# Kernel tuning notes

Measured on AMD Instinct MI355X. Metric: run time of the kernel, lower is better.

Reference implementation:

```python
import jax, jax.numpy as jnp
import numpy as np

DECAY = 0.99
EPS = 1e-5
K = 32  # cluster_size


def setup_inputs() -> dict:
    key = jax.random.key(0)
    k1, k2 = jax.random.split(key)
    B, D, L = 64, 256, 4096
    x = jax.random.normal(k1, (B, D, L), dtype=jnp.float32)
    embed = jax.random.normal(k2, (D, K), dtype=jnp.float32)  # [output_dim, cluster_size]
    cluster_number = jnp.zeros((K,), dtype=jnp.float32)
    embed_avg = embed  # registered buffer initialized as embed.clone()
    return {"x": x, "embed": embed, "cluster_number": cluster_number,
            "embed_avg": embed_avg, "training": 1}


def reference(x, embed, cluster_number, embed_avg, training):
    D = embed.shape[0]
    xt = jnp.transpose(x, (0, 2, 1))          # [B, L, D]
    flatten = xt.reshape(-1, D)               # [N, D]
    # squared L2 distance to each code: ||f||^2 - 2 f.e + ||e||^2
    dist = ((flatten * flatten).sum(1, keepdims=True)
            - 2.0 * flatten @ embed
            + (embed * embed).sum(0, keepdims=True))  # [N, K]
    emb_ind = jnp.argmin(dist, axis=1)        # [N]
    quantize = jnp.take(embed.T, emb_ind, axis=0).reshape(xt.shape)  # [B, L, D]

    if training:
        # EMA codebook update (one-hot sums expressed as segment sums)
        counts = jax.ops.segment_sum(jnp.ones_like(emb_ind, dtype=flatten.dtype),
                                     emb_ind, num_segments=K)          # [K]
        embed_sum = jax.ops.segment_sum(flatten, emb_ind, num_segments=K).T  # [D, K]
        cluster_number = DECAY * cluster_number + (1.0 - DECAY) * counts
        embed_avg = DECAY * embed_avg + (1.0 - DECAY) * embed_sum
        n = cluster_number.sum()
        cn = (cluster_number + EPS) / (n + K * EPS) * n
        embed_out = embed_avg / cn[None, :]
    else:
        embed_out = embed

    discrete_loss = jnp.mean((jax.lax.stop_gradient(quantize) - xt) ** 2)
    quantize = xt + jax.lax.stop_gradient(quantize - xt)  # straight-through
    return jnp.transpose(quantize, (0, 2, 1)), embed_out, discrete_loss
```

## Files before the change

kernel.cpp:

```cpp
#include <hip/hip_runtime.h>


constexpr int   Kc  = 32;
constexpr int   Dc  = 256;
constexpr int   Bc  = 64;
constexpr int   Lc  = 4096;
constexpr int   Nc  = Bc * Lc;
constexpr long  QSIZE = (long)Bc * Dc * Lc;
constexpr float DECAYf = 0.99f;
constexpr float EPSf   = 1e-5f;
constexpr float GAP_THRESH = 0.02f;

constexpr int DCH = 16;
constexpr int NCH = Dc / DCH;

typedef float f32x4 __attribute__((ext_vector_type(4)));

constexpr int WS_LOSS   = 0;
constexpr int WS_COUNTS = 8;
constexpr int NREPC     = 8;
constexpr int WS_ESUM   = 512;

#define WAITVM(N) asm volatile("s_waitcnt vmcnt(" #N ")" ::: "memory")

__device__ __forceinline__ void bar() {
    asm volatile("s_waitcnt lgkmcnt(0)" ::: "memory");
    __builtin_amdgcn_s_barrier();
}

__device__ __forceinline__ void async_ld16(const float* g, float* l) {
    __builtin_amdgcn_global_load_lds(
        (const __attribute__((address_space(1))) void*)g,
        (__attribute__((address_space(3))) void*)l, 16, 0, 0);
}

__device__ __forceinline__ void stage_chunk(const float* xt, int c,
                                            float* sbuf, int tid) {
    const float* g0 = xt + (size_t)(c * DCH) * Lc;
#pragma unroll
    for (int q = 0; q < 4; ++q) {
        const int i4 = q * 256 + tid;
        async_ld16(g0 + (size_t)(i4 >> 6) * Lc + ((i4 & 63) << 2),
                   sbuf + (size_t)i4 * 4);
    }
}

constexpr int SACC    = 4096;
constexpr int SACC_LD = 257;
constexpr int POOLF   = SACC + Kc * SACC_LD;

__global__ __launch_bounds__(256, 3) void vq_main(
    const float* __restrict__ x, const float* __restrict__ embed,
    float* __restrict__ out_q, float* __restrict__ ws, int nrep)
{
    __shared__ float  s_pool[POOLF];
    __shared__ float  s_esq[Kc];
    __shared__ double s_esqd[Kc];
    __shared__ float  s_hist[Kc];
    __shared__ float  s_red[4];
    __shared__ int    s_k[256];

    const int tid = threadIdx.x;
    const int p0  = blockIdx.x * 256;
    const int b   = p0 >> 12;
    const int l0  = p0 & (Lc - 1);
    const float* xt = x + (size_t)b * Dc * Lc + l0;

    stage_chunk(xt, 0, s_pool, tid);

    if (tid < Kc) {
        s_hist[tid] = 0.f;
        double acc = 0.0;
        for (int d = 0; d < Dc; ++d) {
            double e = (double)embed[d * Kc + tid];
            acc = fma(e, e, acc);
        }
        s_esqd[tid] = acc;
        s_esq[tid]  = (float)acc;
    }

    float dot[Kc];
#pragma unroll
    for (int k = 0; k < Kc; ++k) dot[k] = 0.f;
    float xsq = 0.f;

    for (int c = 0; c < NCH; ++c) {
        const int cb = c & 1;
        if (c + 1 < NCH) {
            stage_chunk(xt, c + 1, s_pool + (cb ^ 1) * 4096, tid);
            WAITVM(4);
        } else {
            WAITVM(0);
        }
        bar();
        const float* er0 = embed + c * DCH * Kc;
        const float* sx  = s_pool + cb * 4096;
#pragma unroll
        for (int dd = 0; dd < DCH; ++dd) {
            const float f = sx[dd * 256 + tid];
            xsq = fmaf(f, f, xsq);
            const float* er = er0 + dd * Kc;
#pragma unroll
            for (int k = 0; k < Kc; ++k) dot[k] = fmaf(f, er[k], dot[k]);
        }
        bar();
    }

#pragma unroll
    for (int k = 0; k < Kc; ++k) s_pool[SACC + k * SACC_LD + tid] = 0.f;

    int   kstar  = 0;
    float best   = 3.4e38f;
    float second = 3.4e38f;
#pragma unroll
    for (int k = 0; k < Kc; ++k) {
        float cc = fmaf(-2.0f, dot[k], s_esq[k]);
        if (cc < best)        { second = best; best = cc; kstar = k; }
        else if (cc < second) { second = cc; }
    }

    if (second - best < GAP_THRESH) {
        const float lim = best + GAP_THRESH;
        double bestd = 1e300;
        int kb = 0;
        for (int k = 0; k < Kc; ++k) {
            float cf = fmaf(-2.0f, dot[k], s_esq[k]);
            if (__any(cf <= lim)) {
                double acc = 0.0;
                for (int d = 0; d < Dc; ++d)
                    acc = fma((double)xt[(size_t)d * Lc + tid],
                              (double)embed[d * Kc + k], acc);
                double cc = fma(-2.0, acc, s_esqd[k]);
                if (cc < bestd) { bestd = cc; kb = k; }
            }
        }
        kstar = kb;
    }

    s_k[tid] = kstar;
    atomicAdd(&s_hist[kstar], 1.0f);

    float lacc = best + xsq;
#pragma unroll
    for (int off = 32; off > 0; off >>= 1) lacc += __shfl_down(lacc, off);
    if ((tid & 63) == 0) s_red[tid >> 6] = lacc;
    bar();

    const int repc = blockIdx.x & (NREPC - 1);
    if (tid == 0)
        atomicAdd(&ws[WS_LOSS], s_red[0] + s_red[1] + s_red[2] + s_red[3]);
    if (tid < Kc)
        atomicAdd(&ws[WS_COUNTS + repc * Kc + tid], s_hist[tid]);

    const int rep = blockIdx.x & (nrep - 1);
    float* esum = ws + WS_ESUM + (size_t)rep * Dc * Kc;
    float* ot   = out_q + (size_t)b * Dc * Lc + l0;
    const int w     = tid >> 6;
    const int lane  = tid & 63;
    const int dd_own = tid >> 4;
    const int s_own  = tid & 15;

    int k4[4];
#pragma unroll
    for (int t = 0; t < 4; ++t) k4[t] = s_k[(lane << 2) + t];
    int kk[16];
#pragma unroll
    for (int j = 0; j < 16; ++j) kk[j] = s_k[j * 16 + s_own];

    float* s_acc = s_pool + SACC;

    for (int c = 0; c < NCH; ++c) {
        stage_chunk(xt, c, s_pool, tid);

#pragma unroll
        for (int j = 0; j < 4; ++j) {
            const int d = c * DCH + (j << 2) + w;
            const float* erow = embed + d * Kc;
            f32x4 q;
            q.x = erow[k4[0]];
            q.y = erow[k4[1]];
            q.z = erow[k4[2]];
            q.w = erow[k4[3]];
            __builtin_nontemporal_store(
                q, reinterpret_cast<f32x4*>(ot + (size_t)d * Lc + (lane << 2)));
        }
        WAITVM(0);
        bar();

#pragma unroll
        for (int j = 0; j < 16; ++j) {
            const float f = s_pool[dd_own * 256 + j * 16 + s_own];
            s_acc[kk[j] * SACC_LD + tid] += f;
        }
        bar();

#pragma unroll
        for (int t = 0; t < 2; ++t) {
            const int j2  = (t << 8) + tid;
            const int kc  = j2 & 31;
            const int ddc = j2 >> 5;
            float ssum = 0.f;
#pragma unroll
            for (int s = 0; s < 16; ++s) {
                float* cell = &s_acc[kc * SACC_LD + ddc * 16 + s];
                ssum += *cell;
                *cell = 0.f;
            }
            atomicAdd(&esum[(size_t)(c * DCH + ddc) * Kc + kc], ssum);
        }
        bar();
    }
}

__global__ void vq_finalize(
    const float* __restrict__ embed,
    const float* __restrict__ cluster_number,
    const float* __restrict__ embed_avg,
    const int*   __restrict__ training,
    const float* __restrict__ ws,
    float* __restrict__ out, int nrep)
{
    const int j = blockIdx.x * 256 + threadIdx.x;
    if (j >= Dc * Kc) return;
    const int k = j & (Kc - 1);

    float n = 0.f, cn_k = 0.f;
    for (int kk = 0; kk < Kc; ++kk) {
        float c = 0.f;
        for (int r = 0; r < NREPC; ++r) c += ws[WS_COUNTS + r * Kc + kk];
        float cnew = DECAYf * cluster_number[kk] + (1.0f - DECAYf) * c;
        n += cnew;
        if (kk == k) cn_k = cnew;
    }
    float cn = (cn_k + EPSf) / (n + Kc * EPSf) * n;

    float s = 0.f;
    for (int r = 0; r < nrep; ++r) s += ws[WS_ESUM + (size_t)r * Dc * Kc + j];
    float avg = DECAYf * embed_avg[j] + (1.0f - DECAYf) * s;

    out[QSIZE + j] = (*training) ? (avg / cn) : embed[j];

    if (j == 0) {
        out[QSIZE + Dc * Kc] = ws[WS_LOSS] / (float)QSIZE;
    }
}

extern "C" void kernel_launch(void* const* d_in, const int* in_sizes, int n_in,
                              void* d_out, int out_size, void* d_ws, size_t ws_size,
                              hipStream_t stream)
{
    (void)in_sizes; (void)n_in; (void)out_size;
    const float* x              = (const float*)d_in[0];
    const float* embed          = (const float*)d_in[1];
    const float* cluster_number = (const float*)d_in[2];
    const float* embed_avg      = (const float*)d_in[3];
    const int*   training       = (const int*)d_in[4];
    float* out = (float*)d_out;
    float* ws  = (float*)d_ws;

    const size_t availf = ws_size / 4;
    int nrep = 8;
    while (nrep < 128 &&
           (size_t)WS_ESUM + (size_t)(nrep << 1) * Dc * Kc <= availf)
        nrep <<= 1;

    const size_t used = ((size_t)WS_ESUM + (size_t)nrep * Dc * Kc) * 4;
    (void)hipMemsetAsync(d_ws, 0, used, stream);
    vq_main<<<Nc / 256, 256, 0, stream>>>(x, embed, out, ws, nrep);
    vq_finalize<<<(Dc * Kc + 255) / 256, 256, 0, stream>>>(
        embed, cluster_number, embed_avg, training, ws, out, nrep);
}
```

Before: 628.3 us.

## Restructure scatter pass: direct global x reads, byte-packed indices, smaller LDS for occupancy

The second pass over x no longer stages chunks into LDS asynchronously. Each thread now reads float4 vectors of x straight from global memory and scatters them into the per-code LDS accumulator, working on 32-dim chunks. Code indices are stored as bytes and packed four per dword, which shrinks LDS use and register pressure, and launch bounds rise to 4 blocks per CU. This also drops one barrier per chunk. The risks are uncoalesced-ish direct global reads and a smaller replication count (nrep capped at 64), which means more atomic contention.

```diff
diff --git a/kernel.cpp b/kernel.cpp
--- a/kernel.cpp
+++ b/kernel.cpp
@@ -13,6 +13,8 @@
 
 constexpr int DCH = 16;
 constexpr int NCH = Dc / DCH;
+constexpr int DCH2 = 32;
+constexpr int NCH2 = Dc / DCH2;
 
 typedef float f32x4 __attribute__((ext_vector_type(4)));
 
@@ -45,11 +47,10 @@
     }
 }
 
-constexpr int SACC    = 4096;
 constexpr int SACC_LD = 257;
-constexpr int POOLF   = SACC + Kc * SACC_LD;
-
-__global__ __launch_bounds__(256, 3) void vq_main(
+constexpr int POOLF   = Kc * SACC_LD;
+
+__global__ __launch_bounds__(256, 4) void vq_main(
     const float* __restrict__ x, const float* __restrict__ embed,
     float* __restrict__ out_q, float* __restrict__ ws, int nrep)
 {
@@ -58,7 +59,7 @@
     __shared__ double s_esqd[Kc];
     __shared__ float  s_hist[Kc];
     __shared__ float  s_red[4];
-    __shared__ int    s_k[256];
+    __shared__ unsigned char s_k8[256] __attribute__((aligned(4)));
 
     const int tid = threadIdx.x;
     const int p0  = blockIdx.x * 256;
@@ -107,7 +108,7 @@
     }
 
 #pragma unroll
-    for (int k = 0; k < Kc; ++k) s_pool[SACC + k * SACC_LD + tid] = 0.f;
+    for (int k = 0; k < Kc; ++k) s_pool[k * SACC_LD + tid] = 0.f;
 
     int   kstar  = 0;
     float best   = 3.4e38f;
@@ -137,7 +138,7 @@
         kstar = kb;
     }
 
-    s_k[tid] = kstar;
+    s_k8[tid] = (unsigned char)kstar;
     atomicAdd(&s_hist[kstar], 1.0f);
 
     float lacc = best + xsq;
@@ -155,58 +156,59 @@
     const int rep = blockIdx.x & (nrep - 1);
     float* esum = ws + WS_ESUM + (size_t)rep * Dc * Kc;
     float* ot   = out_q + (size_t)b * Dc * Lc + l0;
-    const int w     = tid >> 6;
-    const int lane  = tid & 63;
-    const int dd_own = tid >> 4;
-    const int s_own  = tid & 15;
-
-    int k4[4];
-#pragma unroll
-    for (int t = 0; t < 4; ++t) k4[t] = s_k[(lane << 2) + t];
-    int kk[16];
-#pragma unroll
-    for (int j = 0; j < 16; ++j) kk[j] = s_k[j * 16 + s_own];
-
-    float* s_acc = s_pool + SACC;
-
-    for (int c = 0; c < NCH; ++c) {
-        stage_chunk(xt, c, s_pool, tid);
-
-#pragma unroll
-        for (int j = 0; j < 4; ++j) {
-            const int d = c * DCH + (j << 2) + w;
+    const int w    = tid >> 6;
+    const int lane = tid & 63;
+    const int dd   = tid >> 3;
+    const int s    = tid & 7;
+
+    const unsigned int k4dw =
+        *reinterpret_cast<const unsigned int*>(s_k8 + 4 * lane);
+    unsigned int kdw[8];
+#pragma unroll
+    for (int j4 = 0; j4 < 8; ++j4)
+        kdw[j4] = *reinterpret_cast<const unsigned int*>(s_k8 + 32 * j4 + 4 * s);
+
+    float* s_acc = s_pool;
+
+    for (int c = 0; c < NCH2; ++c) {
+#pragma unroll
+        for (int j = 0; j < 8; ++j) {
+            const int d = c * DCH2 + (j << 2) + w;
             const float* erow = embed + d * Kc;
             f32x4 q;
-            q.x = erow[k4[0]];
-            q.y = erow[k4[1]];
-            q.z = erow[k4[2]];
-            q.w = erow[k4[3]];
+            q.x = erow[k4dw & 255];
+            q.y = erow[(k4dw >> 8) & 255];
+            q.z = erow[(k4dw >> 16) & 255];
+            q.w = erow[k4dw >> 24];
             __builtin_nontemporal_store(
                 q, reinterpret_cast<f32x4*>(ot + (size_t)d * Lc + (lane << 2)));
         }
-        WAITVM(0);
-        bar();
-
-#pragma unroll
-        for (int j = 0; j < 16; ++j) {
-            const float f = s_pool[dd_own * 256 + j * 16 + s_own];
-            s_acc[kk[j] * SACC_LD + tid] += f;
-        }
-        bar();
-
-#pragma unroll
-        for (int t = 0; t < 2; ++t) {
-            const int j2  = (t << 8) + tid;
-            const int kc  = j2 & 31;
-            const int ddc = j2 >> 5;
+
+        const float* xrow = xt + (size_t)(c * DCH2 + dd) * Lc;
+#pragma unroll
+        for (int j4 = 0; j4 < 8; ++j4) {
+            const f32x4 v = *reinterpret_cast<const f32x4*>(
+                xrow + (j4 << 5) + (s << 2));
+            const unsigned int kw = kdw[j4];
+            s_acc[(kw & 255)         * SACC_LD + tid] += v.x;
+            s_acc[((kw >> 8) & 255)  * SACC_LD + tid] += v.y;
+            s_acc[((kw >> 16) & 255) * SACC_LD + tid] += v.z;
+            s_acc[(kw >> 24)         * SACC_LD + tid] += v.w;
+        }
+        bar();
+
+#pragma unroll
+        for (int i = 0; i < 4; ++i) {
+            const int kc  = tid & 31;
+            const int ddc = (i << 3) + (tid >> 5);
             float ssum = 0.f;
 #pragma unroll
-            for (int s = 0; s < 16; ++s) {
-                float* cell = &s_acc[kc * SACC_LD + ddc * 16 + s];
+            for (int s2 = 0; s2 < 8; ++s2) {
+                float* cell = &s_acc[kc * SACC_LD + (ddc << 3) + s2];
                 ssum += *cell;
                 *cell = 0.f;
             }
-            atomicAdd(&esum[(size_t)(c * DCH + ddc) * Kc + kc], ssum);
+            atomicAdd(&esum[(size_t)(c * DCH2 + ddc) * Kc + kc], ssum);
         }
         bar();
     }
@@ -235,6 +237,7 @@
     float cn = (cn_k + EPSf) / (n + Kc * EPSf) * n;
 
     float s = 0.f;
+#pragma unroll 8
     for (int r = 0; r < nrep; ++r) s += ws[WS_ESUM + (size_t)r * Dc * Kc + j];
     float avg = DECAYf * embed_avg[j] + (1.0f - DECAYf) * s;
 
@@ -260,7 +263,7 @@
 
     const size_t availf = ws_size / 4;
     int nrep = 8;
-    while (nrep < 128 &&
+    while (nrep < 64 &&
            (size_t)WS_ESUM + (size_t)(nrep << 1) * Dc * Kc <= availf)
         nrep <<= 1;
 
```

Result: faster. 588.3 us (-6.4%).
